# Kernel optimization log

Hardware: AMD Instinct MI355X
Metric: run time of the kernel (lower is better)

The kernel has to match this reference:

```python
import jax, jax.numpy as jnp
import numpy as np

TOP_K = 2
CAPACITY_FACTOR = 1.0


def setup_inputs() -> dict:
    key = jax.random.key(0)
    ks = jax.random.split(key, 4)
    sl, bs, hs, ffn, E = 2048, 8, 1024, 4096, 8
    x = jax.random.normal(ks[0], (sl, bs, hs), dtype=jnp.float32)
    w_router = jax.random.normal(ks[1], (hs, E), dtype=jnp.float32) * 0.02
    w1 = jax.random.normal(ks[2], (E, hs, ffn), dtype=jnp.float32) * 0.02
    w2 = jax.random.normal(ks[3], (E, ffn, hs), dtype=jnp.float32) * 0.02
    bias = jnp.zeros((1, 1, hs), dtype=jnp.float32)
    return {"x": x, "w_router": w_router, "w1": w1, "w2": w2, "bias": bias}


def reference(x, w_router, w1, w2, bias):
    sl, bs, hs = x.shape
    E = w_router.shape[1]
    xf = x.reshape(-1, hs)                     # [T, hs]
    T = xf.shape[0]
    capacity = int(CAPACITY_FACTOR * TOP_K * T / E)  # static expert capacity

    # LearnedRouter: softmax over expert logits, then top-k
    scores = jax.nn.softmax(xf @ w_router, axis=-1)          # [T, E]
    expert_weights, top_experts = jax.lax.top_k(scores, TOP_K)

    flat_e = top_experts.reshape(-1)           # [N] N = T*top_k
    flat_w = expert_weights.reshape(-1)
    N = flat_e.shape[0]

    # ops.sort (stable radix sort) + ops.histogram + inclusive_cumsum
    order = jnp.argsort(flat_e, stable=True)   # indices
    bin_ids = flat_e[order]
    tpe = jnp.zeros((E,), jnp.int32).at[flat_e].add(1)       # tokens_per_expert
    starts = jnp.cumsum(tpe) - tpe             # exclusive bin starts
    offsets = jnp.arange(N) - starts[bin_ids]  # position within expert bin

    # binned_gather: first `capacity` tokens per expert, rest dropped
    valid = offsets < capacity
    slot = jnp.where(valid, bin_ids * capacity + offsets, E * capacity)
    src = order // TOP_K                       # source token row for each slot
    xb = jnp.zeros((E * capacity + 1, hs), x.dtype).at[slot].set(xf[src])
    xb = xb[:-1].reshape(E, capacity, hs)

    # grouped MLP (megablocks mlp.MLP): gelu between two grouped GEMMs
    h = jax.nn.gelu(jnp.einsum('ech,ehf->ecf', xb, w1))
    y = jnp.einsum('ecf,efh->ech', h, w2).reshape(E * capacity, hs)

    # binned_scatter: weighted combine back to token order (dropped -> 0)
    yv = jnp.where(valid[:, None], y[jnp.minimum(slot, E * capacity - 1)], 0.0)
    out = jnp.zeros((T, hs), x.dtype).at[src].add(flat_w[order][:, None] * yv)
    return out.reshape(sl, bs, hs) + bias
```

## Files before the change

### kernel.cpp

```cpp
#include <hip/hip_runtime.h>
#include <stdint.h>
#include <math.h>

typedef unsigned short u16;
typedef __attribute__((ext_vector_type(8))) short bf16x8;
typedef __attribute__((ext_vector_type(4))) float f32x4;

#define HS   1024
#define NEXP 8
#define FFN  4096

__device__ __forceinline__ u16 f2b(float f) {
  uint32_t u = __builtin_bit_cast(uint32_t, f);
  u = (u + 0x7fffu + ((u >> 16) & 1u)) >> 16;
  return (u16)u;
}
__device__ __forceinline__ float gelu_tanh(float x) {
  float z = 0.7978845608028654f * (x + 0.044715f * x * x * x);
  float e = __expf(2.0f * z);
  return 0.5f * x * (1.0f + (1.0f - 2.0f / (e + 1.0f)));
}
__device__ __forceinline__ void gload_lds16(const void* g, void* l) {
  __builtin_amdgcn_global_load_lds(
      (__attribute__((address_space(1))) void*)(void*)g,
      (__attribute__((address_space(3))) void*)l, 16, 0, 0);
}

__global__ __launch_bounds__(256) void convert_bf16(const float* __restrict__ in,
                                                    u16* __restrict__ out) {
  const int i = (blockIdx.x * 256 + threadIdx.x) * 4;
  float4 v = *(const float4*)(in + i);
  ushort4 o;
  o.x = f2b(v.x); o.y = f2b(v.y); o.z = f2b(v.z); o.w = f2b(v.w);
  *(ushort4*)(out + i) = o;
}

__global__ __launch_bounds__(256) void transpose_convert(const float* __restrict__ in,
                                                         u16* __restrict__ out,
                                                         int K, int N) {
  __shared__ u16 tile[32][33];
  const int z = blockIdx.z;
  const int k0 = blockIdx.y * 32, n0 = blockIdx.x * 32;
  const int tx = threadIdx.x & 31, ty = threadIdx.x >> 5;
  const float* src = in + (size_t)z * K * N;
  u16* dst = out + (size_t)z * N * K;
#pragma unroll
  for (int i = 0; i < 4; ++i)
    tile[ty + i * 8][tx] = f2b(src[(size_t)(k0 + ty + i * 8) * N + n0 + tx]);
  __syncthreads();
#pragma unroll
  for (int i = 0; i < 4; ++i)
    dst[(size_t)(n0 + ty + i * 8) * K + k0 + tx] = tile[tx][ty + i * 8];
}

__global__ __launch_bounds__(256) void router_kernel(const float* __restrict__ x,
                                                     const float* __restrict__ wr,
                                                     int T, int* __restrict__ experts,
                                                     float* __restrict__ weights) {
  const int wave = threadIdx.x >> 6, lane = threadIdx.x & 63;
  const int t = blockIdx.x * 4 + wave;
  if (t >= T) return;
  const float* xr = x + (size_t)t * HS;
  double acc[8] = {0, 0, 0, 0, 0, 0, 0, 0};
#pragma unroll
  for (int i = 0; i < HS / 64; ++i) {
    const int hrow = i * 64 + lane;
    double xv = (double)xr[hrow];
    float4 w0 = *(const float4*)(wr + hrow * 8);
    float4 w1 = *(const float4*)(wr + hrow * 8 + 4);
    acc[0] += xv * (double)w0.x; acc[1] += xv * (double)w0.y;
    acc[2] += xv * (double)w0.z; acc[3] += xv * (double)w0.w;
    acc[4] += xv * (double)w1.x; acc[5] += xv * (double)w1.y;
    acc[6] += xv * (double)w1.z; acc[7] += xv * (double)w1.w;
  }
#pragma unroll
  for (int e = 0; e < 8; ++e) {
    double v = acc[e];
#pragma unroll
    for (int off = 32; off > 0; off >>= 1) v += __shfl_xor(v, off, 64);
    acc[e] = v;
  }
  if (lane == 0) {
    double m = acc[0];
#pragma unroll
    for (int e = 1; e < 8; ++e) m = acc[e] > m ? acc[e] : m;
    double s[8], sum = 0.0;
#pragma unroll
    for (int e = 0; e < 8; ++e) { s[e] = exp(acc[e] - m); sum += s[e]; }
    double inv = 1.0 / sum;
    int e1 = 0; double l1 = acc[0];
#pragma unroll
    for (int e = 1; e < 8; ++e) if (acc[e] > l1) { l1 = acc[e]; e1 = e; }
    int e2 = -1; double l2 = -1e300;
#pragma unroll
    for (int e = 0; e < 8; ++e) if (e != e1 && acc[e] > l2) { l2 = acc[e]; e2 = e; }
    experts[2 * t] = e1;  experts[2 * t + 1] = e2;
    weights[2 * t] = (float)(s[e1] * inv);
    weights[2 * t + 1] = (float)(s[e2] * inv);
  }
}

__global__ __launch_bounds__(256) void hist_kernel(const int* __restrict__ experts,
                                                   int* __restrict__ hist,
                                                   unsigned char* __restrict__ lrank) {
  const int n = blockIdx.x * 256 + threadIdx.x;
  const int lane = threadIdx.x & 63;
  const int wid = n >> 6;
  const int e = experts[n];
  int rank = 0;
#pragma unroll
  for (int ev = 0; ev < 8; ++ev) {
    unsigned long long m = __ballot(e == ev);
    if (lane == ev) hist[wid * 8 + ev] = __popcll(m);
    if (e == ev) rank = __popcll(m & ((1ull << lane) - 1ull));
  }
  lrank[n] = (unsigned char)rank;
}

__global__ __launch_bounds__(512) void scan_kernel(const int* __restrict__ hist,
                                                   int* __restrict__ chunkBase) {
  __shared__ int s[512];
  const int tid = threadIdx.x;
  for (int e = 0; e < 8; ++e) {
    int v = hist[tid * 8 + e];
    s[tid] = v;
    __syncthreads();
    for (int off = 1; off < 512; off <<= 1) {
      int add = (tid >= off) ? s[tid - off] : 0;
      __syncthreads();
      s[tid] += add;
      __syncthreads();
    }
    chunkBase[tid * 8 + e] = s[tid] - v;
    __syncthreads();
  }
}

__global__ __launch_bounds__(256) void slot_init(int* __restrict__ rowtok,
                                                 float* __restrict__ roww) {
  const int i = blockIdx.x * 256 + threadIdx.x;
  rowtok[i] = -1;
  roww[i] = 0.0f;
}

__global__ __launch_bounds__(256) void gather_kernel(const float* __restrict__ x,
                                                     const int* __restrict__ experts,
                                                     const unsigned char* __restrict__ lrank,
                                                     const int* __restrict__ chunkBase,
                                                     const float* __restrict__ weights,
                                                     int capacity, int* __restrict__ rowtok,
                                                     float* __restrict__ roww,
                                                     u16* __restrict__ xb) {
  const int wave = threadIdx.x >> 6, lane = threadIdx.x & 63;
  const int n = blockIdx.x * 4 + wave;
  const int e = experts[n];
  const int off = chunkBase[(n >> 6) * 8 + e] + (int)lrank[n];
  if (off >= capacity) return;
  const int slot = e * capacity + off;
  if (lane == 0) { rowtok[slot] = n >> 1; roww[slot] = weights[n]; }
  if (xb == nullptr) return;
  const float* src = x + (size_t)(n >> 1) * HS;
  u16* dst = xb + (size_t)slot * HS;
#pragma unroll
  for (int i = 0; i < 4; ++i) {
    float4 v = *(const float4*)(src + i * 256 + lane * 4);
    ushort4 o;
    o.x = f2b(v.x); o.y = f2b(v.y); o.z = f2b(v.z); o.w = f2b(v.w);
    *(ushort4*)(dst + i * 256 + lane * 4) = o;
  }
}

__global__ __launch_bounds__(256) void bias_init(const float* __restrict__ bias,
                                                 float* __restrict__ out) {
  const int c = threadIdx.x * 4;
  *(float4*)(out + (size_t)blockIdx.x * HS + c) = *(const float4*)(bias + c);
}

#define VMCNT(n) asm volatile("s_waitcnt vmcnt(" #n ")" ::: "memory")
#define BAR() do { asm volatile("" ::: "memory"); \
                   __builtin_amdgcn_s_barrier();  \
                   asm volatile("" ::: "memory"); } while (0)

template <bool GELU, bool GATHER_A, bool SCATTER>
__global__ __launch_bounds__(512, 2) void gemm_moe(const u16* __restrict__ A,
                                                   const u16* __restrict__ Bt,
                                                   u16* __restrict__ Cout,
                                                   float* __restrict__ out,
                                                   const int* __restrict__ rowtok,
                                                   const float* __restrict__ roww,
                                                   int rtStride, int M, int Nn, int K) {
  const int z = blockIdx.z;
  const int bm = blockIdx.y, bn = blockIdx.x;
  if (!GATHER_A) A += (size_t)z * M * K;
  Bt += (size_t)z * Nn * K;
  rowtok += (size_t)z * rtStride;
  roww += (size_t)z * rtStride;
  const u16* Bb = Bt + (size_t)bn * 256 * K;

  __shared__ u16 lds[65536];
  char* ldsA = (char*)lds;
  char* ldsB = ldsA + 65536;

  const int tid = threadIdx.x;
  const int lane = tid & 63;
  const int lrow = lane & 15, quad = lane >> 4;
  const int wid = tid >> 6, wm = wid >> 2, wn = wid & 3;

  const int swz = (lane & 7) << 4;
  const int kq0 = (quad * 16) ^ swz;
  const int kq1 = (64 + quad * 16) ^ swz;
  const int aBase = (wm * 128 + lrow) * 128;
  const int bBase = (wn * 64 + lrow) * 128;

  const u16 *gA[4], *gB[4];
#pragma unroll
  for (int s = 0; s < 4; ++s) {
    const int srow = s * 64 + (tid >> 3);
    const int scol = ((tid & 7) * 8) ^ ((srow & 7) << 3);
    if (GATHER_A) {
      int t = rowtok[bm * 256 + srow]; if (t < 0) t = 0;
      gA[s] = A + (size_t)t * K + scol;
    } else {
      gA[s] = A + (size_t)(bm * 256 + srow) * K + scol;
    }
    gB[s] = Bb + (size_t)srow * K + scol;
  }
  const int ldst0 = tid * 16;

#define STAGE_A(buf, half, kt) do { \
    gload_lds16(gA[(half)*2]   + (size_t)(kt) * 64, ldsA + (buf)*32768 + (half)*16384 +        ldst0); \
    gload_lds16(gA[(half)*2+1] + (size_t)(kt) * 64, ldsA + (buf)*32768 + (half)*16384 + 8192 + ldst0); \
  } while (0)
#define STAGE_B(buf, half, kt) do { \
    gload_lds16(gB[(half)*2]   + (size_t)(kt) * 64, ldsB + (buf)*32768 + (half)*16384 +        ldst0); \
    gload_lds16(gB[(half)*2+1] + (size_t)(kt) * 64, ldsB + (buf)*32768 + (half)*16384 + 8192 + ldst0); \
  } while (0)

  f32x4 acc[8][4] = {};
  bf16x8 a[8][2];

#define LOAD_A(ABUF) \
  _Pragma("unroll") \
  for (int m = 0; m < 8; ++m) { \
    a[m][0] = *(const bf16x8*)((ABUF) + aBase + m * 2048 + kq0); \
    a[m][1] = *(const bf16x8*)((ABUF) + aBase + m * 2048 + kq1); \
  }

#define PHASE(BBUF, NF, STAGE_STMT, TAIL_STMT) do { \
    bf16x8 b0 = *(const bf16x8*)((BBUF) + bBase + (NF) * 2048 + kq0); \
    bf16x8 b1 = *(const bf16x8*)((BBUF) + bBase + (NF) * 2048 + kq1); \
    STAGE_STMT; \
    BAR(); \
    __builtin_amdgcn_s_setprio(1); \
    _Pragma("unroll") \
    for (int m = 0; m < 8; ++m) { \
      acc[m][NF] = __builtin_amdgcn_mfma_f32_16x16x32_bf16(a[m][0], b0, acc[m][NF], 0, 0, 0); \
      acc[m][NF] = __builtin_amdgcn_mfma_f32_16x16x32_bf16(a[m][1], b1, acc[m][NF], 0, 0, 0); \
    } \
    __builtin_amdgcn_s_setprio(0); \
    TAIL_STMT; \
    BAR(); \
  } while (0)

  STAGE_A(0, 0, 0); STAGE_A(0, 1, 0);
  STAGE_B(0, 0, 0); STAGE_B(0, 1, 0);
  STAGE_A(1, 0, 1); STAGE_A(1, 1, 1);
  VMCNT(4);
  BAR();

  const int nIter = K >> 7;
  for (int I = 0; I < nIter; ++I) {
    const int T1 = 2 * I + 1;
    const bool hn = (I + 1 < nIter);
    LOAD_A(ldsA);
    PHASE(ldsB, 0, STAGE_B(1, 0, T1), ((void)0));
    PHASE(ldsB, 1, STAGE_B(1, 1, T1), ((void)0));
    PHASE(ldsB, 2, do { if (hn) STAGE_A(0, 0, T1 + 1); } while (0), ((void)0));
    PHASE(ldsB, 3, do { if (hn) STAGE_A(0, 1, T1 + 1); } while (0),
          do { if (hn) { VMCNT(4); } else { VMCNT(0); } } while (0));
    LOAD_A(ldsA + 32768);
    PHASE(ldsB + 32768, 0, do { if (hn) STAGE_B(0, 0, T1 + 1); } while (0), ((void)0));
    PHASE(ldsB + 32768, 1, do { if (hn) STAGE_B(0, 1, T1 + 1); } while (0), ((void)0));
    PHASE(ldsB + 32768, 2, do { if (hn) STAGE_A(1, 0, T1 + 2); } while (0), ((void)0));
    PHASE(ldsB + 32768, 3, do { if (hn) STAGE_A(1, 1, T1 + 2); } while (0),
          do { if (hn) { VMCNT(4); } } while (0));
  }

  const int rbase = bm * 256 + wm * 128 + quad * 4;
  const int cbase = bn * 256 + wn * 64 + lrow;
  if (!SCATTER) {
    u16* Cb = Cout + (size_t)z * M * Nn;
#pragma unroll
    for (int m = 0; m < 8; ++m)
#pragma unroll
      for (int nf = 0; nf < 4; ++nf)
#pragma unroll
        for (int r = 0; r < 4; ++r) {
          float v = acc[m][nf][r];
          if (GELU) v = gelu_tanh(v);
          Cb[(size_t)(rbase + m * 16 + r) * Nn + cbase + nf * 16] = f2b(v);
        }
  } else {
#pragma unroll
    for (int m = 0; m < 8; ++m)
#pragma unroll
      for (int r = 0; r < 4; ++r) {
        const int row = rbase + m * 16 + r;
        const int tok = rowtok[row];
        if (tok >= 0) {
          const float w = roww[row];
          float* op = out + (size_t)tok * HS + cbase;
#pragma unroll
          for (int nf = 0; nf < 4; ++nf)
            atomicAdd(op + nf * 16, w * acc[m][nf][r]);
        }
      }
  }
}

extern "C" void kernel_launch(void* const* d_in, const int* in_sizes, int n_in,
                              void* d_out, int out_size, void* d_ws, size_t ws_size,
                              hipStream_t stream) {
  const float* x    = (const float*)d_in[0];
  const float* wr   = (const float*)d_in[1];
  const float* w1   = (const float*)d_in[2];
  const float* w2   = (const float*)d_in[3];
  const float* bias = (const float*)d_in[4];
  float* out = (float*)d_out;

  const int T = in_sizes[0] / HS;
  const int N = T * 2;
  const int capacity = N / NEXP;
  const int nChunks = N / 64;

  char* ws = (char*)d_ws;
  int* experts = (int*)ws;                   ws += (size_t)N * 4;
  float* weights = (float*)ws;               ws += (size_t)N * 4;
  unsigned char* lrank = (unsigned char*)ws; ws += (size_t)N;
  int* hist = (int*)ws;                      ws += (size_t)nChunks * 8 * 4;
  int* chunkBase = (int*)ws;                 ws += (size_t)nChunks * 8 * 4;
  int* rowtok = (int*)ws;                    ws += (size_t)NEXP * capacity * 4;
  float* roww = (float*)ws;                  ws += (size_t)NEXP * capacity * 4;
  ws = (char*)(((uintptr_t)ws + 255) & ~(uintptr_t)255);
  size_t used = (size_t)(ws - (char*)d_ws);
  size_t avail = ws_size > used ? ws_size - used : 0;

  const size_t xbB  = (size_t)NEXP * capacity * HS * 2;
  const size_t perE = ((size_t)FFN * HS * 2) * 2 + (size_t)capacity * FFN * 2;

  int G = 0;
  for (int g = NEXP; g >= 1; g >>= 1)
    if (avail >= xbB + (size_t)g * perE) { G = g; break; }

  u16 *xb = nullptr, *xbf = nullptr, *w1t, *w2t, *h;
  if (G > 0) {
    xb  = (u16*)ws;  ws += xbB;
    w1t = (u16*)ws;  ws += (size_t)G * FFN * HS * 2;
    w2t = (u16*)ws;  ws += (size_t)G * HS * FFN * 2;
    h   = (u16*)ws;  ws += (size_t)G * capacity * FFN * 2;
  } else {
    G = 1;
    xbf = (u16*)ws;  ws += (size_t)T * HS * 2;
    w1t = (u16*)ws;  ws += (size_t)FFN * HS * 2;
    w2t = (u16*)ws;  ws += (size_t)HS * FFN * 2;
    h   = (u16*)ws;  ws += (size_t)capacity * FFN * 2;
    if ((size_t)(ws - (char*)d_ws) > ws_size) return;
    convert_bf16<<<T * HS / 1024, 256, 0, stream>>>(x, xbf);
  }

  router_kernel<<<T / 4, 256, 0, stream>>>(x, wr, T, experts, weights);
  hist_kernel<<<N / 256, 256, 0, stream>>>(experts, hist, lrank);
  scan_kernel<<<1, 512, 0, stream>>>(hist, chunkBase);
  slot_init<<<NEXP * capacity / 256, 256, 0, stream>>>(rowtok, roww);
  gather_kernel<<<N / 4, 256, 0, stream>>>(x, experts, lrank, chunkBase, weights,
                                           capacity, rowtok, roww, xb);
  bias_init<<<T, 256, 0, stream>>>(bias, out);

  for (int e0 = 0; e0 < NEXP; e0 += G) {
    const float* w1_g = w1 + (size_t)e0 * HS * FFN;
    const float* w2_g = w2 + (size_t)e0 * FFN * HS;
    const int* rt_g = rowtok + e0 * capacity;
    const float* rw_g = roww + e0 * capacity;
    transpose_convert<<<dim3(FFN / 32, HS / 32, G), 256, 0, stream>>>(w1_g, w1t, HS, FFN);
    transpose_convert<<<dim3(HS / 32, FFN / 32, G), 256, 0, stream>>>(w2_g, w2t, FFN, HS);
    if (xb != nullptr) {
      gemm_moe<true, false, false><<<dim3(FFN / 256, capacity / 256, G), 512, 0, stream>>>(
          xb + (size_t)e0 * capacity * HS, w1t, h, nullptr, rt_g, rw_g,
          capacity, capacity, FFN, HS);
    } else {
      gemm_moe<true, true, false><<<dim3(FFN / 256, capacity / 256, G), 512, 0, stream>>>(
          xbf, w1t, h, nullptr, rt_g, rw_g, capacity, capacity, FFN, HS);
    }
    gemm_moe<false, false, true><<<dim3(HS / 256, capacity / 256, G), 512, 0, stream>>>(
        h, w2t, nullptr, out, rt_g, rw_g, capacity, capacity, HS, FFN);
  }
}
```

Before: 1.088 ms.

## Remap GEMM workgroups per XCD with column grouping and drop per-phase trailing barriers

Workgroup IDs are remapped so that consecutive tiles land on the same XCD. Tiles are also grouped into bands of four N-columns, so blocks that share weight and activation tiles tend to hit the same L2. Separately, the trailing barrier after each MFMA phase is removed, keeping only the one at the end of each half-iteration after the vmcnt wait. This cuts barrier stalls per K-step. The risk is an LDS write-after-read hazard if a staged load overwrites data another wave is still reading.

```diff
diff --git a/kernel.cpp b/kernel.cpp
--- a/kernel.cpp
+++ b/kernel.cpp
@@ -189,8 +189,26 @@
                                                    const int* __restrict__ rowtok,
                                                    const float* __restrict__ roww,
                                                    int rtStride, int M, int Nn, int K) {
-  const int z = blockIdx.z;
-  const int bm = blockIdx.y, bn = blockIdx.x;
+  int bn, bm, z;
+  {
+    const int gx = gridDim.x, gy = gridDim.y, gz = gridDim.z;
+    const int nwg = gx * gy * gz;
+    const int flat = (blockIdx.z * gy + blockIdx.y) * gx + blockIdx.x;
+    const int q = nwg >> 3, r = nwg & 7;
+    const int xcd = flat & 7, idx = flat >> 3;
+    const int base = (xcd < r) ? xcd * (q + 1) : r * (q + 1) + (xcd - r) * q;
+    int nid = base + idx;
+    const int perz = gx * gy;
+    z = nid / perz;
+    int rem = nid - z * perz;
+    const int GN = (gx >= 4) ? 4 : gx;
+    const int grpsz = GN * gy;
+    const int grp = rem / grpsz, ir = rem - grp * grpsz;
+    const int bnl = ir % GN;
+    bm = ir / GN;
+    bn = grp * GN + bnl;
+  }
+
   if (!GATHER_A) A += (size_t)z * M * K;
   Bt += (size_t)z * Nn * K;
   rowtok += (size_t)z * rtStride;
@@ -246,20 +264,19 @@
     a[m][1] = *(const bf16x8*)((ABUF) + aBase + m * 2048 + kq1); \
   }
 
-#define PHASE(BBUF, NF, STAGE_STMT, TAIL_STMT) do { \
-    bf16x8 b0 = *(const bf16x8*)((BBUF) + bBase + (NF) * 2048 + kq0); \
-    bf16x8 b1 = *(const bf16x8*)((BBUF) + bBase + (NF) * 2048 + kq1); \
+#define PHASE(BBUF, NF, STAGE_STMT, END_STMT) do { \
+    bf16x8 pb0 = *(const bf16x8*)((BBUF) + bBase + (NF) * 2048 + kq0); \
+    bf16x8 pb1 = *(const bf16x8*)((BBUF) + bBase + (NF) * 2048 + kq1); \
     STAGE_STMT; \
     BAR(); \
     __builtin_amdgcn_s_setprio(1); \
     _Pragma("unroll") \
     for (int m = 0; m < 8; ++m) { \
-      acc[m][NF] = __builtin_amdgcn_mfma_f32_16x16x32_bf16(a[m][0], b0, acc[m][NF], 0, 0, 0); \
-      acc[m][NF] = __builtin_amdgcn_mfma_f32_16x16x32_bf16(a[m][1], b1, acc[m][NF], 0, 0, 0); \
+      acc[m][NF] = __builtin_amdgcn_mfma_f32_16x16x32_bf16(a[m][0], pb0, acc[m][NF], 0, 0, 0); \
+      acc[m][NF] = __builtin_amdgcn_mfma_f32_16x16x32_bf16(a[m][1], pb1, acc[m][NF], 0, 0, 0); \
     } \
     __builtin_amdgcn_s_setprio(0); \
-    TAIL_STMT; \
-    BAR(); \
+    END_STMT; \
   } while (0)
 
   STAGE_A(0, 0, 0); STAGE_A(0, 1, 0);
@@ -277,13 +294,13 @@
     PHASE(ldsB, 1, STAGE_B(1, 1, T1), ((void)0));
     PHASE(ldsB, 2, do { if (hn) STAGE_A(0, 0, T1 + 1); } while (0), ((void)0));
     PHASE(ldsB, 3, do { if (hn) STAGE_A(0, 1, T1 + 1); } while (0),
-          do { if (hn) { VMCNT(4); } else { VMCNT(0); } } while (0));
+          do { if (hn) { VMCNT(4); } else { VMCNT(0); } BAR(); } while (0));
     LOAD_A(ldsA + 32768);
     PHASE(ldsB + 32768, 0, do { if (hn) STAGE_B(0, 0, T1 + 1); } while (0), ((void)0));
     PHASE(ldsB + 32768, 1, do { if (hn) STAGE_B(0, 1, T1 + 1); } while (0), ((void)0));
     PHASE(ldsB + 32768, 2, do { if (hn) STAGE_A(1, 0, T1 + 2); } while (0), ((void)0));
     PHASE(ldsB + 32768, 3, do { if (hn) STAGE_A(1, 1, T1 + 2); } while (0),
-          do { if (hn) { VMCNT(4); } } while (0));
+          do { if (hn) { VMCNT(4); } BAR(); } while (0));
   }
 
   const int rbase = bm * 256 + wm * 128 + quad * 4;
```

New measurement: 1.044 ms. 1.04x faster.
